# Kernel tuning notes

Hardware: AMD Instinct MI355X
Metric: run time of the kernel (lower is better)

Reference implementation:

```python
import jax, jax.numpy as jnp
import numpy as np

B, T, H, NEX, ED = 65536, 20, 10, 13, 3

def _p(k, shape):
    return (jax.random.normal(k, shape, jnp.float32) * 0.1)

def setup_inputs() -> dict:
    key = jax.random.key(0)
    ks = jax.random.split(key, 24)
    e = jax.random.randint(ks[0], (B, T), 0, NEX, dtype=jnp.int32)
    f = jax.random.normal(ks[1], (B, T, 3), jnp.float32)
    emb = _p(ks[2], (NEX, ED)).at[0].set(0.0)  # row 0 zeroed as in torch init
    feat_w = _p(ks[3], (3, 3))
    feat_b = _p(ks[4], (3,))
    d = {"e": e, "f": f, "emb": emb, "feat_w": feat_w, "feat_b": feat_b}
    i = 5
    for layer, insz in ((0, 6), (1, 2 * H)):
        for sfx in ("", "r"):
            d[f"w_ih_l{layer}{sfx}"] = _p(ks[i], (4 * H, insz)); i += 1
            d[f"w_hh_l{layer}{sfx}"] = _p(ks[i], (4 * H, H)); i += 1
            d[f"b_ih_l{layer}{sfx}"] = _p(ks[i], (4 * H,)); i += 1
            d[f"b_hh_l{layer}{sfx}"] = _p(ks[i], (4 * H,)); i += 1
    return d

def _lstm_dir(x, w_ih, w_hh, b_ih, b_hh, reverse):
    # x: (B, T, I) -> hidden sequence (B, T, H). PyTorch gate order: i, f, g, o.
    xs = jnp.swapaxes(x, 0, 1)                      # (T, B, I)
    pre = xs @ w_ih.T + (b_ih + b_hh)               # input contribution, (T, B, 4H)
    def step(carry, p):
        h, c = carry
        g = p + h @ w_hh.T
        i, fg, gg, o = jnp.split(g, 4, axis=-1)
        c = jax.nn.sigmoid(fg) * c + jax.nn.sigmoid(i) * jnp.tanh(gg)
        h = jax.nn.sigmoid(o) * jnp.tanh(c)
        return (h, c), h
    nb = x.shape[0]
    init = (jnp.zeros((nb, H), x.dtype), jnp.zeros((nb, H), x.dtype))
    _, hs = jax.lax.scan(step, init, pre, reverse=reverse)
    return jnp.swapaxes(hs, 0, 1)                   # (B, T, H)

def _bilstm_layer(x, pf, pb):
    hf = _lstm_dir(x, *pf, reverse=False)
    hb = _lstm_dir(x, *pb, reverse=True)
    return jnp.concatenate([hf, hb], axis=-1)       # (B, T, 2H)

def reference(e, f, emb, feat_w, feat_b,
              w_ih_l0, w_hh_l0, b_ih_l0, b_hh_l0,
              w_ih_l0r, w_hh_l0r, b_ih_l0r, b_hh_l0r,
              w_ih_l1, w_hh_l1, b_ih_l1, b_hh_l1,
              w_ih_l1r, w_hh_l1r, b_ih_l1r, b_hh_l1r):
    ev = emb[e]                                     # (B, T, 3)
    f3 = f.reshape(-1, T, 3)
    mask = (f3[:, :, 1] != 0).astype(f.dtype)       # (B, T)
    fv = f3 @ feat_w.T + feat_b                     # (B, T, 3)
    x = jnp.concatenate([ev, fv], axis=2)           # (B, T, 6)
    x = _bilstm_layer(x, (w_ih_l0, w_hh_l0, b_ih_l0, b_hh_l0),
                         (w_ih_l0r, w_hh_l0r, b_ih_l0r, b_hh_l0r))
    x = _bilstm_layer(x, (w_ih_l1, w_hh_l1, b_ih_l1, b_hh_l1),
                         (w_ih_l1r, w_hh_l1r, b_ih_l1r, b_hh_l1r))
    ipe = jax.nn.relu(x[:, :, -1] * mask)           # last channel = backward dir unit H-1
    total = ipe.sum(axis=1, keepdims=True)          # (B, 1)
    return (total, ipe)
```

## Files before the change

kernel.cpp:

```cpp
#include <hip/hip_runtime.h>

#define BB 65536
#define TT 20
#define NG16 4096
#define FR_ROW 160

#define WS_AF  0
#define WS_OLD 2304
#define WS_FR  8192
#define PKB 0x00003C00u

#define LOG2E  1.442695041f
#define LOG2E2 2.885390082f

typedef unsigned u32;
typedef __fp16 f16x8 __attribute__((ext_vector_type(8)));
typedef float   f32x16 __attribute__((ext_vector_type(16)));
typedef float   f32x4v __attribute__((ext_vector_type(4)));
typedef u32     u32x4 __attribute__((ext_vector_type(4)));
typedef __fp16  h2v   __attribute__((ext_vector_type(2)));

__device__ __forceinline__ u32 pk_h16(float a, float b) {
    h2v v = __builtin_amdgcn_cvt_pkrtz(a, b);
    return __builtin_bit_cast(u32, v);
}
__device__ __forceinline__ f32x4v MFMA16(u32x4 a, u32x4 b, f32x4v c) {
    return __builtin_amdgcn_mfma_f32_16x16x32_f16(
        __builtin_bit_cast(f16x8, a), __builtin_bit_cast(f16x8, b), c, 0, 0, 0);
}
__device__ __forceinline__ f32x16 MFMA32(u32x4 a, u32x4 b, f32x16 c) {
    return __builtin_amdgcn_mfma_f32_32x32x16_f16(
        __builtin_bit_cast(f16x8, a), __builtin_bit_cast(f16x8, b), c, 0, 0, 0);
}

__device__ __forceinline__ void unit_cr(float ai, float af, float ag, float ao,
                                        float* c, float* h) {
    float pi = __builtin_amdgcn_exp2f(-LOG2E * ai);
    float pf = __builtin_amdgcn_exp2f(-LOG2E * af);
    float q  = __builtin_amdgcn_exp2f(LOG2E2 * ag);
    float fv = __builtin_amdgcn_rcpf(1.0f + pf);
    float ig = (q - 1.0f) * __builtin_amdgcn_rcpf((1.0f + pi) * (q + 1.0f));
    float cv = fmaf(fv, *c, ig);
    *c = cv;
    float po = __builtin_amdgcn_exp2f(-LOG2E * ao);
    float qc = __builtin_amdgcn_exp2f(LOG2E2 * cv);
    *h = (qc - 1.0f) * __builtin_amdgcn_rcpf((1.0f + po) * (qc + 1.0f));
}

__global__ __launch_bounds__(256)
void prep16(
    const float* __restrict__ wih0, const float* __restrict__ whh0,
    const float* __restrict__ bih0, const float* __restrict__ bhh0,
    const float* __restrict__ wih0r,const float* __restrict__ whh0r,
    const float* __restrict__ bih0r,const float* __restrict__ bhh0r,
    const float* __restrict__ wih1r,const float* __restrict__ whh1r,
    const float* __restrict__ bih1r,const float* __restrict__ bhh1r,
    u32* __restrict__ ws)
{
    for (int gid = threadIdx.x; gid < 9 * 64 * 4; gid += 256) {
        int fid = gid >> 8;
        int ct = fid / 3, T = fid % 3;
        int l = (gid >> 2) & 63, j = gid & 3;
        int m = l & 15, qq = l >> 4;
        int mq = m >> 2, gate = m & 3;
        int unit;
        if (T == 0)      unit = 2 * mq;
        else if (T == 1) unit = 2 * mq + 1;
        else             unit = (mq < 2) ? (8 + mq) : 99;
        float v[2] = {0.f, 0.f};
        if (unit <= 9) {
            int orow = gate * 10 + unit;
#pragma unroll
            for (int s = 0; s < 2; ++s) {
                int k = (j >> 1) * 16 + 4 * qq + (j & 1) * 2 + s;
                float val = 0.f;
                if (ct < 2) {
                    const float* wih = ct ? wih0r : wih0;
                    const float* whh = ct ? whh0r : whh0;
                    if (k < 6)            val = wih[orow * 6 + k];
                    else if (k == 6)      val = ct ? (bih0r[orow] + bhh0r[orow])
                                               : (bih0[orow] + bhh0[orow]);
                    else if (k >= 8 && k <= 17) val = whh[orow * 10 + (k - 8)];
                } else {
                    if (k < 20)           val = wih1r[orow * 20 + k];
                    else if (k <= 29)     val = whh1r[orow * 10 + (k - 20)];
                    else if (k == 30)     val = bih1r[orow] + bhh1r[orow];
                }
                v[s] = val;
            }
        }
        ws[WS_AF + (fid * 64 + l) * 4 + j] = pk_h16(v[0], v[1]);
    }
}

struct Lds16 {
    u32   bx[4][TT][16][4];
    float m[4][TT][16];
    u32   hx[4][2][16][6];
    u32   zpad[2];
};

__global__ __launch_bounds__(256, 4)
void bilstm16(
    const int*   __restrict__ eidx, const float* __restrict__ f,
    const float* __restrict__ emb,  const float* __restrict__ fw,
    const float* __restrict__ fb,
    const u32* __restrict__ wsr, u32* __restrict__ fr,
    float* __restrict__ out)
{
    __shared__ Lds16 lds;
    const int tid  = threadIdx.x;
    const int lane = tid & 63;
    const int e    = lane & 15;
    const int q    = lane >> 4;
    const int wv   = __builtin_amdgcn_readfirstlane(tid >> 6);
    const int g    = blockIdx.x * 4 + wv;
    const int b0   = g * 16;
    const int xaddr16 = (e + 16) << 2;
    u32* frp = fr + (size_t)g * TT * FR_ROW;

    {
        float fw0=fw[0],fw1=fw[1],fw2=fw[2],fw3=fw[3],fw4=fw[4];
        float fw5=fw[5],fw6=fw[6],fw7=fw[7],fw8=fw[8];
        float fb0=fb[0],fb1=fb[1],fb2=fb[2];
#pragma unroll 1
        for (int it = 0; it < 5; ++it) {
            int idx = lane + it * 64;
            int ee = idx / TT, t = idx - ee * TT;
            int gi = (b0 + ee) * TT + t;
            float f0 = f[gi * 3], f1 = f[gi * 3 + 1], f2v = f[gi * 3 + 2];
            int ei = eidx[gi] * 3;
            float x0 = emb[ei], x1 = emb[ei + 1], x2 = emb[ei + 2];
            float x3 = fmaf(fw0, f0, fmaf(fw1, f1, fmaf(fw2, f2v, fb0)));
            float x4 = fmaf(fw3, f0, fmaf(fw4, f1, fmaf(fw5, f2v, fb1)));
            float x5 = fmaf(fw6, f0, fmaf(fw7, f1, fmaf(fw8, f2v, fb2)));
            lds.bx[wv][t][ee][0] = pk_h16(x0, x1);
            lds.bx[wv][t][ee][1] = pk_h16(x2, x3);
            lds.bx[wv][t][ee][2] = pk_h16(x4, x5);
            lds.bx[wv][t][ee][3] = PKB;
            lds.m[wv][t][ee]     = (f1 != 0.f) ? 1.f : 0.f;
        }
        u32* zz = &lds.hx[wv][0][0][0];
        zz[lane] = 0u; zz[lane + 64] = 0u; zz[lane + 128] = 0u;
        if (lane < 2) lds.zpad[lane] = 0u;
    }

    u32* hxF = &lds.hx[wv][0][e][0];
    u32* hxB = &lds.hx[wv][1][e][0];
    const u32* zp = lds.zpad;
    const u32x4* wv4 = (const u32x4*)(wsr + WS_AF);
    const f32x4v z4 = {};

    {
        u32x4 F0 = wv4[0 * 64 + lane], F1 = wv4[1 * 64 + lane], F2 = wv4[2 * 64 + lane];
        u32x4 G0 = wv4[3 * 64 + lane], G1 = wv4[4 * 64 + lane], G2 = wv4[5 * 64 + lane];
        const u32* aF  = (q < 2) ? &lds.bx[wv][0][e][2 * q]      : &hxF[2 * (q - 2)];
        const u32* aB  = (q < 2) ? &lds.bx[wv][TT - 1][e][2 * q] : &hxB[2 * (q - 2)];
        const u32* a2F = (q == 0) ? &hxF[4] : zp;
        const u32* a2B = (q == 0) ? &hxB[4] : zp;
        const int  strA = (q < 2) ? 64 : 0;

        float cF[3] = {0,0,0}, cB[3] = {0,0,0};
#pragma unroll 1
        for (int s = 0; s < TT; ++s) {
            u32x4 bf; bf[0] = aF[s * strA]; bf[1] = aF[s * strA + 1];
            bf[2] = *a2F; bf[3] = 0u;
            f32x4v A0 = MFMA16(F0, bf, z4), A1 = MFMA16(F1, bf, z4), A2 = MFMA16(F2, bf, z4);
            u32x4 bb; bb[0] = aB[-s * strA]; bb[1] = aB[-s * strA + 1];
            bb[2] = *a2B; bb[3] = 0u;
            f32x4v C0 = MFMA16(G0, bb, z4), C1 = MFMA16(G1, bb, z4), C2 = MFMA16(G2, bb, z4);
            float hF[3], hB[3];
            unit_cr(A0[0], A0[1], A0[2], A0[3], &cF[0], &hF[0]);
            unit_cr(A1[0], A1[1], A1[2], A1[3], &cF[1], &hF[1]);
            unit_cr(A2[0], A2[1], A2[2], A2[3], &cF[2], &hF[2]);
            unit_cr(C0[0], C0[1], C0[2], C0[3], &cB[0], &hB[0]);
            unit_cr(C1[0], C1[1], C1[2], C1[3], &cB[1], &hB[1]);
            unit_cr(C2[0], C2[1], C2[2], C2[3], &cB[2], &hB[2]);
            u32 pF = pk_h16(hF[0], hF[1]);
            u32 pB = pk_h16(hB[0], hB[1]);
            hxF[q] = pF;
            hxB[q] = pB;
            u32 rF = (u32)__builtin_amdgcn_ds_bpermute(xaddr16, (int)__float_as_uint(hF[2]));
            u32 rB = (u32)__builtin_amdgcn_ds_bpermute(xaddr16, (int)__float_as_uint(hB[2]));
            u32 s4F = pk_h16(hF[2], __uint_as_float(rF));
            u32 s4B = pk_h16(hB[2], __uint_as_float(rB));
            if (q == 0) { hxF[4] = s4F; hxB[4] = s4B; }
            u32* frT = frp + s * FR_ROW;
            u32* frB = frp + (TT - 1 - s) * FR_ROW;
            frT[e * 10 + q]     = pF;
            frB[e * 10 + 5 + q] = pB;
            if (q == 0) {
                frT[e * 10 + 4] = s4F;
                frB[e * 10 + 9] = s4B;
            }
        }
    }

    {
        u32x4 H0 = wv4[6 * 64 + lane], H1 = wv4[7 * 64 + lane], H2 = wv4[8 * 64 + lane];
        u32* hz = &lds.hx[wv][0][0][0];
        hz[lane] = 0u;
        if (lane < 32) hz[64 + lane] = 0u;
        const u32* caddr = (q == 0) ? zp : &lds.hx[wv][0][e][2 * (q - 1)];
        const int loffA = e * 10 + q * 2;
        const int loffB = e * 10 + 8;
        float cH[3] = {0,0,0}, tot = 0.f;
        u32 La0 = frp[(TT - 1) * FR_ROW + loffA], La1 = frp[(TT - 1) * FR_ROW + loffA + 1];
        u32 Lb0 = frp[(TT - 1) * FR_ROW + loffB], Lb1 = frp[(TT - 1) * FR_ROW + loffB + 1];
#pragma unroll 1
        for (int t = TT - 1; t >= 0; --t) {
            u32 c0 = caddr[0], c1 = caddr[1];
            u32x4 bc;
            bc[0] = La0;
            bc[1] = La1;
            bc[2] = (q == 0) ? Lb0 : c0;
            bc[3] = (q == 0) ? Lb1 : ((q == 3) ? PKB : c1);
            if (t > 0) {
                La0 = frp[(t - 1) * FR_ROW + loffA]; La1 = frp[(t - 1) * FR_ROW + loffA + 1];
                Lb0 = frp[(t - 1) * FR_ROW + loffB]; Lb1 = frp[(t - 1) * FR_ROW + loffB + 1];
            }
            f32x4v D0 = MFMA16(H0, bc, z4), D1 = MFMA16(H1, bc, z4), D2 = MFMA16(H2, bc, z4);
            float hH[3];
            unit_cr(D0[0], D0[1], D0[2], D0[3], &cH[0], &hH[0]);
            unit_cr(D1[0], D1[1], D1[2], D1[3], &cH[1], &hH[1]);
            unit_cr(D2[0], D2[1], D2[2], D2[3], &cH[2], &hH[2]);
            u32 pH = pk_h16(hH[0], hH[1]);
            hxF[q] = pH;
            u32 rH = (u32)__builtin_amdgcn_ds_bpermute(xaddr16, (int)__float_as_uint(hH[2]));
            if (q == 0) hxF[4] = pk_h16(hH[2], __uint_as_float(rH));
            if (q == 1) {
                float ip = fmaxf(hH[2] * lds.m[wv][t][e], 0.f);
                out[BB + (b0 + e) * TT + t] = ip;
                tot += ip;
            }
        }
        if (q == 1) out[b0 + e] = tot;
    }
}

__device__ __forceinline__ u32x4 pack_h32(const float* h, bool hi, int xaddr, u32 b3) {
    u32 send = hi ? pk_h16(h[3], h[4]) : __float_as_uint(h[4]);
    u32 recv = (u32)__builtin_amdgcn_ds_bpermute(xaddr, (int)send);
    u32 lo0 = pk_h16(h[0], h[1]), lo1 = pk_h16(h[2], h[3]);
    u32 hi0 = pk_h16(__uint_as_float(recv), h[0]);
    u32 hi1 = pk_h16(h[1], h[2]);
    u32x4 b;
    b[0] = hi ? hi0 : lo0; b[1] = hi ? hi1 : lo1;
    b[2] = hi ? 0u : recv; b[3] = b3;
    return b;
}
__device__ __forceinline__ void cell_update5(const f32x16 a0, const f32x16 a1,
                                             float* c, float* h) {
#pragma unroll
    for (int v = 0; v < 4; ++v)
        unit_cr(a0[v], a0[4 + v], a0[8 + v], a0[12 + v], &c[v], &h[v]);
    unit_cr(a1[0], a1[1], a1[2], a1[3], &c[4], &h[4]);
}
__device__ __forceinline__ int inv_pi(int row) {
    if (row < 32) { int q = row >> 3, rem = row & 7; return q * 10 + 5 * (rem >> 2) + (rem & 3); }
    if (row < 40) { int lo = row - 32; return (lo & 3) * 10 + 5 * (lo >> 2) + 4; }
    return -1;
}
__global__ __launch_bounds__(256)
void prep_old(
    const float* __restrict__ wih0, const float* __restrict__ whh0,
    const float* __restrict__ bih0, const float* __restrict__ bhh0,
    const float* __restrict__ wih0r,const float* __restrict__ whh0r,
    const float* __restrict__ bih0r,const float* __restrict__ bhh0r,
    const float* __restrict__ wih1r,const float* __restrict__ whh1r,
    const float* __restrict__ bih1r,const float* __restrict__ bhh1r,
    u32* __restrict__ ws)
{
    for (int gid = threadIdx.x; gid < 14 * 64 * 4; gid += 256) {
        int fid = gid >> 8, l = (gid >> 2) & 63, j = gid & 3;
        int gq = l >> 5;
        int tile, chunk;
        if (fid < 8) { tile = (fid >> 1) & 1; chunk = fid & 1; }
        else         { int q2 = fid - 8; tile = q2 / 3; chunk = q2 % 3; }
        int row = tile * 32 + (l & 31);
        int orow = inv_pi(row);
        int kb = (j >> 1) * 8 + 4 * gq + (j & 1) * 2;
        float v[2] = {0.f, 0.f};
        if (orow >= 0) {
#pragma unroll
            for (int s = 0; s < 2; ++s) {
                int k = kb + s;
                float val = 0.f;
                if (fid < 8) {
                    bool bwd = fid >= 4;
                    if (chunk == 0) {
                        if (k < 6)       val = (bwd ? wih0r : wih0)[orow * 6 + k];
                        else if (k == 6) val = (bwd ? bih0r[orow] + bhh0r[orow]
                                                    : bih0[orow] + bhh0[orow]);
                    } else { if (k < 10) val = (bwd ? whh0r : whh0)[orow * 10 + k]; }
                } else {
                    if (chunk == 0)      { if (k < 10) val = wih1r[orow * 20 + k]; }
                    else if (chunk == 1) { if (k < 10) val = wih1r[orow * 20 + 10 + k]; }
                    else {
                        if (k < 10)       val = whh1r[orow * 10 + k];
                        else if (k == 10) val = bih1r[orow] + bhh1r[orow];
                    }
                }
                v[s] = val;
            }
        }
        ws[WS_OLD + (fid * 64 + l) * 4 + j] = pk_h16(v[0], v[1]);
    }
}
struct LdsFB { u32 x[TT][3][32]; float m[TT][32]; u32 hf[TT][160]; };
__global__ __launch_bounds__(64)
void bilstm_fb(
    const int*   __restrict__ eidx, const float* __restrict__ f,
    const float* __restrict__ emb,  const float* __restrict__ fw,
    const float* __restrict__ fb,
    const u32* __restrict__ wsr, float* __restrict__ out)
{
    __shared__ LdsFB lds;
    const int  lane = threadIdx.x;
    const int  e    = lane & 31;
    const bool hi   = lane >= 32;
    const int  wid  = blockIdx.x;
    const int  b0   = wid * 32;
    const int  xaddr = (lane ^ 32) << 2;
    {
        float fw0=fw[0],fw1=fw[1],fw2=fw[2],fw3=fw[3],fw4=fw[4];
        float fw5=fw[5],fw6=fw[6],fw7=fw[7],fw8=fw[8];
        float fb0=fb[0],fb1=fb[1],fb2=fb[2];
#pragma unroll 1
        for (int it = 0; it < 10; ++it) {
            int idx = lane + it * 64;
            int ee = idx / 20, t = idx - ee * 20;
            int gi = (b0 + ee) * TT + t;
            float f0 = f[gi * 3], f1 = f[gi * 3 + 1], f2v = f[gi * 3 + 2];
            int ei = eidx[gi] * 3;
            float x0 = emb[ei], x1 = emb[ei + 1], x2 = emb[ei + 2];
            float x3 = fmaf(fw0, f0, fmaf(fw1, f1, fmaf(fw2, f2v, fb0)));
            float x4 = fmaf(fw3, f0, fmaf(fw4, f1, fmaf(fw5, f2v, fb1)));
            float x5 = fmaf(fw6, f0, fmaf(fw7, f1, fmaf(fw8, f2v, fb2)));
            lds.x[t][0][ee] = pk_h16(x0, x1);
            lds.x[t][1][ee] = pk_h16(x2, x3);
            lds.x[t][2][ee] = pk_h16(x4, x5);
            lds.m[t][ee]    = (f1 != 0.f) ? 1.f : 0.f;
        }
    }
    const u32x4* wv = (const u32x4*)(wsr + WS_OLD);
    const f32x16 zf = {};
    {
        u32x4 wf0 = wv[0 * 64 + lane], wf1 = wv[1 * 64 + lane];
        u32x4 wf2 = wv[2 * 64 + lane], wf3 = wv[3 * 64 + lane];
        float cf[5] = {0,0,0,0,0}, hv[5] = {0,0,0,0,0};
        u32x4 bx0;
        {
            u32 x01 = lds.x[0][0][e], x23 = lds.x[0][1][e], x45 = lds.x[0][2][e];
            bx0[0] = hi ? x45 : x01; bx0[1] = hi ? PKB : x23; bx0[2] = 0u; bx0[3] = 0u;
        }
        f32x16 a0x = MFMA32(wf0, bx0, zf);
        f32x16 a1x = MFMA32(wf2, bx0, zf);
        u32x4 bh;
#pragma unroll 1
        for (int t = 0; t < TT; ++t) {
            f32x16 a0 = a0x, a1 = a1x;
            if (t > 0) { a0 = MFMA32(wf1, bh, a0); a1 = MFMA32(wf3, bh, a1); }
            if (t + 1 < TT) {
                u32 x01 = lds.x[t+1][0][e], x23 = lds.x[t+1][1][e], x45 = lds.x[t+1][2][e];
                u32x4 bx; bx[0] = hi ? x45 : x01; bx[1] = hi ? PKB : x23; bx[2] = 0u; bx[3] = 0u;
                a0x = MFMA32(wf0, bx, zf);
                a1x = MFMA32(wf2, bx, zf);
            }
            cell_update5(a0, a1, cf, hv);
            bh = pack_h32(hv, hi, xaddr, 0u);
            lds.hf[t][lane * 2] = bh[0]; lds.hf[t][lane * 2 + 1] = bh[1];
            if (!hi) lds.hf[t][128 + e] = bh[2];
        }
    }
    {
        u32x4 wb0 = wv[4 * 64 + lane], wb1 = wv[5 * 64 + lane];
        u32x4 wb2 = wv[6 * 64 + lane], wb3 = wv[7 * 64 + lane];
        u32x4 wB0 = wv[8 * 64 + lane], wB1 = wv[9 * 64 + lane], wB2 = wv[10 * 64 + lane];
        u32x4 wB3 = wv[11 * 64 + lane], wB4 = wv[12 * 64 + lane], wB5 = wv[13 * 64 + lane];
        float cb[5] = {0,0,0,0,0}, hbv[5] = {0,0,0,0,0};
        float cc[5] = {0,0,0,0,0}, h1v[5] = {0,0,0,0,0};
        float tot = 0.f;
        {
            u32 x01 = lds.x[TT-1][0][e], x23 = lds.x[TT-1][1][e], x45 = lds.x[TT-1][2][e];
            u32x4 bx; bx[0] = hi ? x45 : x01; bx[1] = hi ? PKB : x23; bx[2] = 0u; bx[3] = 0u;
            f32x16 a0 = MFMA32(wb0, bx, zf);
            f32x16 a1 = MFMA32(wb2, bx, zf);
            cell_update5(a0, a1, cb, hbv);
        }
        uint2 cur2 = make_uint2(lds.hf[TT-1][lane * 2], lds.hf[TT-1][lane * 2 + 1]);
        u32   curw = lds.hf[TT-1][128 + e];
#pragma unroll 1
        for (int t = TT - 1; t >= 1; --t) {
            uint2 nxt2 = make_uint2(lds.hf[t-1][lane * 2], lds.hf[t-1][lane * 2 + 1]);
            u32   nxtw = lds.hf[t-1][128 + e];
            u32x4 shared = pack_h32(hbv, hi, xaddr, 0u);
            u32x4 bh1    = pack_h32(h1v, hi, xaddr, hi ? 0u : PKB);
            u32x4 bhf; bhf[0] = cur2.x; bhf[1] = cur2.y; bhf[2] = hi ? 0u : curw; bhf[3] = 0u;
            f32x16 B0 = MFMA32(wB0, bhf, zf); B0 = MFMA32(wB1, shared, B0); B0 = MFMA32(wB2, bh1, B0);
            f32x16 B1 = MFMA32(wB3, bhf, zf); B1 = MFMA32(wB4, shared, B1); B1 = MFMA32(wB5, bh1, B1);
            u32 x01 = lds.x[t-1][0][e], x23 = lds.x[t-1][1][e], x45 = lds.x[t-1][2][e];
            u32x4 bx; bx[0] = hi ? x45 : x01; bx[1] = hi ? PKB : x23; bx[2] = 0u; bx[3] = 0u;
            f32x16 A0 = MFMA32(wb0, bx, zf); A0 = MFMA32(wb1, shared, A0);
            f32x16 A1 = MFMA32(wb2, bx, zf); A1 = MFMA32(wb3, shared, A1);
            cell_update5(B0, B1, cc, h1v);
            if (hi) {
                float ip = fmaxf(h1v[4] * lds.m[t][e], 0.f);
                out[BB + (b0 + e) * TT + t] = ip;
                tot += ip;
            }
            cell_update5(A0, A1, cb, hbv);
            cur2 = nxt2; curw = nxtw;
        }
        {
            u32x4 shared = pack_h32(hbv, hi, xaddr, 0u);
            u32x4 bh1    = pack_h32(h1v, hi, xaddr, hi ? 0u : PKB);
            u32x4 bhf; bhf[0] = cur2.x; bhf[1] = cur2.y; bhf[2] = hi ? 0u : curw; bhf[3] = 0u;
            f32x16 B0 = MFMA32(wB0, bhf, zf); B0 = MFMA32(wB1, shared, B0); B0 = MFMA32(wB2, bh1, B0);
            f32x16 B1 = MFMA32(wB3, bhf, zf); B1 = MFMA32(wB4, shared, B1); B1 = MFMA32(wB5, bh1, B1);
            cell_update5(B0, B1, cc, h1v);
            if (hi) {
                float ip = fmaxf(h1v[4] * lds.m[0][e], 0.f);
                out[BB + (b0 + e) * TT + 0] = ip;
                tot += ip;
                out[b0 + e] = tot;
            }
        }
    }
}

extern "C" void kernel_launch(void* const* d_in, const int* in_sizes, int n_in,
                              void* d_out, int out_size, void* d_ws, size_t ws_size,
                              hipStream_t stream) {
    const int*   eidx  = (const int*)  d_in[0];
    const float* f     = (const float*)d_in[1];
    const float* emb   = (const float*)d_in[2];
    const float* fw    = (const float*)d_in[3];
    const float* fb    = (const float*)d_in[4];
    const float* wih0  = (const float*)d_in[5];
    const float* whh0  = (const float*)d_in[6];
    const float* bih0  = (const float*)d_in[7];
    const float* bhh0  = (const float*)d_in[8];
    const float* wih0r = (const float*)d_in[9];
    const float* whh0r = (const float*)d_in[10];
    const float* bih0r = (const float*)d_in[11];
    const float* bhh0r = (const float*)d_in[12];
    const float* wih1r = (const float*)d_in[17];
    const float* whh1r = (const float*)d_in[18];
    const float* bih1r = (const float*)d_in[19];
    const float* bhh1r = (const float*)d_in[20];
    float* out = (float*)d_out;
    u32* ws = (u32*)d_ws;

    const size_t need16 = (size_t)(WS_FR + (size_t)NG16 * TT * FR_ROW + 64) * 4;
    if (ws_size >= need16) {
        hipLaunchKernelGGL(prep16, dim3(1), dim3(256), 0, stream,
                           wih0, whh0, bih0, bhh0, wih0r, whh0r, bih0r, bhh0r,
                           wih1r, whh1r, bih1r, bhh1r, ws);
        hipLaunchKernelGGL(bilstm16, dim3(NG16 / 4), dim3(256), 0, stream,
                           eidx, f, emb, fw, fb, ws, ws + WS_FR, out);
    } else {
        hipLaunchKernelGGL(prep_old, dim3(1), dim3(256), 0, stream,
                           wih0, whh0, bih0, bhh0, wih0r, whh0r, bih0r, bhh0r,
                           wih1r, whh1r, bih1r, bhh1r, ws);
        hipLaunchKernelGGL(bilstm_fb, dim3(BB / 32), dim3(64), 0, stream,
                           eidx, f, emb, fw, fb, ws, out);
    }
}
```

Measured before the change: 72.30 us.

## Split forward and backward layer-0 directions across separate waves per group

Each block now handles two 16-sequence groups with four waves. Two waves run the forward layer-0 recurrence and two run the backward one, instead of one wave doing both directions in an interleaved loop. After a block barrier, the first two waves run the layer-1 backward recurrence for their group, which leaves half the waves idle during that phase. The aim is to shorten the serial dependency chain per wave and raise occupancy (launch bounds 8). The cost is less instruction-level parallelism per wave, an extra __syncthreads, and idle waves in layer 1.

```diff
diff --git a/kernel.cpp b/kernel.cpp
--- a/kernel.cpp
+++ b/kernel.cpp
@@ -93,120 +93,119 @@
     }
 }
 
-struct Lds16 {
-    u32   bx[4][TT][16][4];
-    float m[4][TT][16];
-    u32   hx[4][2][16][6];
+struct Lds8 {
+    u32   bx[2][TT][16][4];
+    float m[2][TT][16];
+    u32   hx[2][2][16][6];
     u32   zpad[2];
 };
 
-__global__ __launch_bounds__(256, 4)
-void bilstm16(
+__global__ __launch_bounds__(256, 8)
+void bilstm8(
     const int*   __restrict__ eidx, const float* __restrict__ f,
     const float* __restrict__ emb,  const float* __restrict__ fw,
     const float* __restrict__ fb,
     const u32* __restrict__ wsr, u32* __restrict__ fr,
     float* __restrict__ out)
 {
-    __shared__ Lds16 lds;
+    __shared__ Lds8 lds;
     const int tid  = threadIdx.x;
     const int lane = tid & 63;
     const int e    = lane & 15;
     const int q    = lane >> 4;
-    const int wv   = __builtin_amdgcn_readfirstlane(tid >> 6);
-    const int g    = blockIdx.x * 4 + wv;
-    const int b0   = g * 16;
+    const int wu   = __builtin_amdgcn_readfirstlane(tid >> 6);
+    const int role = wu >> 1;
+    const int gl   = wu & 1;
+    const int g    = blockIdx.x * 2 + gl;
     const int xaddr16 = (e + 16) << 2;
-    u32* frp = fr + (size_t)g * TT * FR_ROW;
 
     {
         float fw0=fw[0],fw1=fw[1],fw2=fw[2],fw3=fw[3],fw4=fw[4];
         float fw5=fw[5],fw6=fw[6],fw7=fw[7],fw8=fw[8];
         float fb0=fb[0],fb1=fb[1],fb2=fb[2];
 #pragma unroll 1
-        for (int it = 0; it < 5; ++it) {
-            int idx = lane + it * 64;
-            int ee = idx / TT, t = idx - ee * TT;
-            int gi = (b0 + ee) * TT + t;
-            float f0 = f[gi * 3], f1 = f[gi * 3 + 1], f2v = f[gi * 3 + 2];
-            int ei = eidx[gi] * 3;
-            float x0 = emb[ei], x1 = emb[ei + 1], x2 = emb[ei + 2];
-            float x3 = fmaf(fw0, f0, fmaf(fw1, f1, fmaf(fw2, f2v, fb0)));
-            float x4 = fmaf(fw3, f0, fmaf(fw4, f1, fmaf(fw5, f2v, fb1)));
-            float x5 = fmaf(fw6, f0, fmaf(fw7, f1, fmaf(fw8, f2v, fb2)));
-            lds.bx[wv][t][ee][0] = pk_h16(x0, x1);
-            lds.bx[wv][t][ee][1] = pk_h16(x2, x3);
-            lds.bx[wv][t][ee][2] = pk_h16(x4, x5);
-            lds.bx[wv][t][ee][3] = PKB;
-            lds.m[wv][t][ee]     = (f1 != 0.f) ? 1.f : 0.f;
-        }
-        u32* zz = &lds.hx[wv][0][0][0];
-        zz[lane] = 0u; zz[lane + 64] = 0u; zz[lane + 128] = 0u;
-        if (lane < 2) lds.zpad[lane] = 0u;
-    }
-
-    u32* hxF = &lds.hx[wv][0][e][0];
-    u32* hxB = &lds.hx[wv][1][e][0];
+        for (int it = 0; it < 3; ++it) {
+            int idx = tid + it * 256;
+            if (idx < 640) {
+                int gg = idx / 320, rem = idx - gg * 320;
+                int ee = rem / TT, t = rem - ee * TT;
+                int gi = ((blockIdx.x * 2 + gg) * 16 + ee) * TT + t;
+                float f0 = f[gi * 3], f1 = f[gi * 3 + 1], f2v = f[gi * 3 + 2];
+                int ei = eidx[gi] * 3;
+                float x0 = emb[ei], x1 = emb[ei + 1], x2 = emb[ei + 2];
+                float x3 = fmaf(fw0, f0, fmaf(fw1, f1, fmaf(fw2, f2v, fb0)));
+                float x4 = fmaf(fw3, f0, fmaf(fw4, f1, fmaf(fw5, f2v, fb1)));
+                float x5 = fmaf(fw6, f0, fmaf(fw7, f1, fmaf(fw8, f2v, fb2)));
+                lds.bx[gg][t][ee][0] = pk_h16(x0, x1);
+                lds.bx[gg][t][ee][1] = pk_h16(x2, x3);
+                lds.bx[gg][t][ee][2] = pk_h16(x4, x5);
+                lds.bx[gg][t][ee][3] = PKB;
+                lds.m[gg][t][ee]     = (f1 != 0.f) ? 1.f : 0.f;
+            }
+        }
+        u32* zz = &lds.hx[0][0][0][0];
+        zz[tid & 255] = 0u;
+        if (tid < 128) zz[256 + tid] = 0u;
+        if (tid < 2) lds.zpad[tid] = 0u;
+    }
+    __syncthreads();
+
     const u32* zp = lds.zpad;
     const u32x4* wv4 = (const u32x4*)(wsr + WS_AF);
     const f32x4v z4 = {};
+    u32* frp = fr + (size_t)g * TT * FR_ROW;
 
     {
-        u32x4 F0 = wv4[0 * 64 + lane], F1 = wv4[1 * 64 + lane], F2 = wv4[2 * 64 + lane];
-        u32x4 G0 = wv4[3 * 64 + lane], G1 = wv4[4 * 64 + lane], G2 = wv4[5 * 64 + lane];
-        const u32* aF  = (q < 2) ? &lds.bx[wv][0][e][2 * q]      : &hxF[2 * (q - 2)];
-        const u32* aB  = (q < 2) ? &lds.bx[wv][TT - 1][e][2 * q] : &hxB[2 * (q - 2)];
-        const u32* a2F = (q == 0) ? &hxF[4] : zp;
-        const u32* a2B = (q == 0) ? &hxB[4] : zp;
-        const int  strA = (q < 2) ? 64 : 0;
-
-        float cF[3] = {0,0,0}, cB[3] = {0,0,0};
+        const int wb = role * 3;
+        u32x4 W0 = wv4[(wb + 0) * 64 + lane];
+        u32x4 W1 = wv4[(wb + 1) * 64 + lane];
+        u32x4 W2 = wv4[(wb + 2) * 64 + lane];
+        u32* hxO = &lds.hx[gl][role][e][0];
+        const int t0   = role ? TT - 1 : 0;
+        const int sdir = role ? -1 : 1;
+        const u32* aX  = (q < 2) ? &lds.bx[gl][t0][e][2 * q] : &hxO[2 * (q - 2)];
+        const u32* a2  = (q == 0) ? &hxO[4] : zp;
+        const int  strA = (q < 2) ? sdir * 64 : 0;
+        u32* pMain = frp + t0 * FR_ROW + e * 10 + role * 5 + q;
+        u32* pXtra = frp + t0 * FR_ROW + e * 10 + role * 5 + 4;
+        const int strF = sdir * FR_ROW;
+
+        float cS[3] = {0,0,0};
 #pragma unroll 1
         for (int s = 0; s < TT; ++s) {
-            u32x4 bf; bf[0] = aF[s * strA]; bf[1] = aF[s * strA + 1];
-            bf[2] = *a2F; bf[3] = 0u;
-            f32x4v A0 = MFMA16(F0, bf, z4), A1 = MFMA16(F1, bf, z4), A2 = MFMA16(F2, bf, z4);
-            u32x4 bb; bb[0] = aB[-s * strA]; bb[1] = aB[-s * strA + 1];
-            bb[2] = *a2B; bb[3] = 0u;
-            f32x4v C0 = MFMA16(G0, bb, z4), C1 = MFMA16(G1, bb, z4), C2 = MFMA16(G2, bb, z4);
-            float hF[3], hB[3];
-            unit_cr(A0[0], A0[1], A0[2], A0[3], &cF[0], &hF[0]);
-            unit_cr(A1[0], A1[1], A1[2], A1[3], &cF[1], &hF[1]);
-            unit_cr(A2[0], A2[1], A2[2], A2[3], &cF[2], &hF[2]);
-            unit_cr(C0[0], C0[1], C0[2], C0[3], &cB[0], &hB[0]);
-            unit_cr(C1[0], C1[1], C1[2], C1[3], &cB[1], &hB[1]);
-            unit_cr(C2[0], C2[1], C2[2], C2[3], &cB[2], &hB[2]);
-            u32 pF = pk_h16(hF[0], hF[1]);
-            u32 pB = pk_h16(hB[0], hB[1]);
-            hxF[q] = pF;
-            hxB[q] = pB;
-            u32 rF = (u32)__builtin_amdgcn_ds_bpermute(xaddr16, (int)__float_as_uint(hF[2]));
-            u32 rB = (u32)__builtin_amdgcn_ds_bpermute(xaddr16, (int)__float_as_uint(hB[2]));
-            u32 s4F = pk_h16(hF[2], __uint_as_float(rF));
-            u32 s4B = pk_h16(hB[2], __uint_as_float(rB));
-            if (q == 0) { hxF[4] = s4F; hxB[4] = s4B; }
-            u32* frT = frp + s * FR_ROW;
-            u32* frB = frp + (TT - 1 - s) * FR_ROW;
-            frT[e * 10 + q]     = pF;
-            frB[e * 10 + 5 + q] = pB;
-            if (q == 0) {
-                frT[e * 10 + 4] = s4F;
-                frB[e * 10 + 9] = s4B;
-            }
-        }
-    }
-
-    {
+            u32x4 b; b[0] = aX[0]; b[1] = aX[1]; b[2] = *a2; b[3] = 0u;
+            f32x4v A0 = MFMA16(W0, b, z4), A1 = MFMA16(W1, b, z4), A2 = MFMA16(W2, b, z4);
+            float h0, h1, h2;
+            unit_cr(A0[0], A0[1], A0[2], A0[3], &cS[0], &h0);
+            unit_cr(A1[0], A1[1], A1[2], A1[3], &cS[1], &h1);
+            unit_cr(A2[0], A2[1], A2[2], A2[3], &cS[2], &h2);
+            u32 pP = pk_h16(h0, h1);
+            hxO[q] = pP;
+            u32 r9 = (u32)__builtin_amdgcn_ds_bpermute(xaddr16, (int)__float_as_uint(h2));
+            u32 s4 = pk_h16(h2, __uint_as_float(r9));
+            if (q == 0) hxO[4] = s4;
+            *pMain = pP;
+            if (q == 0) *pXtra = s4;
+            aX += strA; pMain += strF; pXtra += strF;
+        }
+    }
+    __syncthreads();
+
+    if (wu < 2) {
+        const int gB = blockIdx.x * 2 + wu;
+        const int b0 = gB * 16;
+        u32* frB = fr + (size_t)gB * TT * FR_ROW;
         u32x4 H0 = wv4[6 * 64 + lane], H1 = wv4[7 * 64 + lane], H2 = wv4[8 * 64 + lane];
-        u32* hz = &lds.hx[wv][0][0][0];
+        u32* hx1 = &lds.hx[wu][0][e][0];
+        u32* hz = &lds.hx[wu][0][0][0];
         hz[lane] = 0u;
         if (lane < 32) hz[64 + lane] = 0u;
-        const u32* caddr = (q == 0) ? zp : &lds.hx[wv][0][e][2 * (q - 1)];
+        const u32* caddr = (q == 0) ? zp : &lds.hx[wu][0][e][2 * (q - 1)];
         const int loffA = e * 10 + q * 2;
         const int loffB = e * 10 + 8;
         float cH[3] = {0,0,0}, tot = 0.f;
-        u32 La0 = frp[(TT - 1) * FR_ROW + loffA], La1 = frp[(TT - 1) * FR_ROW + loffA + 1];
-        u32 Lb0 = frp[(TT - 1) * FR_ROW + loffB], Lb1 = frp[(TT - 1) * FR_ROW + loffB + 1];
+        u32 La0 = frB[(TT - 1) * FR_ROW + loffA], La1 = frB[(TT - 1) * FR_ROW + loffA + 1];
+        u32 Lb0 = frB[(TT - 1) * FR_ROW + loffB], Lb1 = frB[(TT - 1) * FR_ROW + loffB + 1];
 #pragma unroll 1
         for (int t = TT - 1; t >= 0; --t) {
             u32 c0 = caddr[0], c1 = caddr[1];
@@ -216,20 +215,19 @@
             bc[2] = (q == 0) ? Lb0 : c0;
             bc[3] = (q == 0) ? Lb1 : ((q == 3) ? PKB : c1);
             if (t > 0) {
-                La0 = frp[(t - 1) * FR_ROW + loffA]; La1 = frp[(t - 1) * FR_ROW + loffA + 1];
-                Lb0 = frp[(t - 1) * FR_ROW + loffB]; Lb1 = frp[(t - 1) * FR_ROW + loffB + 1];
+                La0 = frB[(t - 1) * FR_ROW + loffA]; La1 = frB[(t - 1) * FR_ROW + loffA + 1];
+                Lb0 = frB[(t - 1) * FR_ROW + loffB]; Lb1 = frB[(t - 1) * FR_ROW + loffB + 1];
             }
             f32x4v D0 = MFMA16(H0, bc, z4), D1 = MFMA16(H1, bc, z4), D2 = MFMA16(H2, bc, z4);
-            float hH[3];
-            unit_cr(D0[0], D0[1], D0[2], D0[3], &cH[0], &hH[0]);
-            unit_cr(D1[0], D1[1], D1[2], D1[3], &cH[1], &hH[1]);
-            unit_cr(D2[0], D2[1], D2[2], D2[3], &cH[2], &hH[2]);
-            u32 pH = pk_h16(hH[0], hH[1]);
-            hxF[q] = pH;
-            u32 rH = (u32)__builtin_amdgcn_ds_bpermute(xaddr16, (int)__float_as_uint(hH[2]));
-            if (q == 0) hxF[4] = pk_h16(hH[2], __uint_as_float(rH));
+            float h0, h1, h2;
+            unit_cr(D0[0], D0[1], D0[2], D0[3], &cH[0], &h0);
+            unit_cr(D1[0], D1[1], D1[2], D1[3], &cH[1], &h1);
+            unit_cr(D2[0], D2[1], D2[2], D2[3], &cH[2], &h2);
+            hx1[q] = pk_h16(h0, h1);
+            u32 rH = (u32)__builtin_amdgcn_ds_bpermute(xaddr16, (int)__float_as_uint(h2));
+            if (q == 0) hx1[4] = pk_h16(h2, __uint_as_float(rH));
             if (q == 1) {
-                float ip = fmaxf(hH[2] * lds.m[wv][t][e], 0.f);
+                float ip = fmaxf(h2 * lds.m[wu][t][e], 0.f);
                 out[BB + (b0 + e) * TT + t] = ip;
                 tot += ip;
             }
@@ -457,7 +455,7 @@
         hipLaunchKernelGGL(prep16, dim3(1), dim3(256), 0, stream,
                            wih0, whh0, bih0, bhh0, wih0r, whh0r, bih0r, bhh0r,
                            wih1r, whh1r, bih1r, bhh1r, ws);
-        hipLaunchKernelGGL(bilstm16, dim3(NG16 / 4), dim3(256), 0, stream,
+        hipLaunchKernelGGL(bilstm8, dim3(NG16 / 2), dim3(256), 0, stream,
                            eidx, f, emb, fw, fb, ws, ws + WS_FR, out);
     } else {
         hipLaunchKernelGGL(prep_old, dim3(1), dim3(256), 0, stream,
```

Result: slower. 74.11 us (+2.5%).
